# Performance work log

Hardware: AMD Instinct MI355X
Metric: run time of the kernel (lower is better)

The kernel has to match this reference:

```python
import jax, jax.numpy as jnp
import numpy as np
from jax import lax

DIM = 256
HEADS = 8
SR = 4
EPS = 1e-5
SCALE = (DIM // HEADS) ** -0.5


def _dwconv(x, wgt, stride, pad):
    # x: (B,C,H,W), wgt: (C,1,kh,kw) depthwise
    return lax.conv_general_dilated(
        x, wgt, (stride, stride), [(pad, pad), (pad, pad)],
        feature_group_count=x.shape[1],
        dimension_numbers=("NCHW", "OIHW", "NCHW"))


def _bn(x, g, b, m, v):
    # eval-mode batchnorm folded to per-channel scale/shift
    s = g / jnp.sqrt(v + EPS)
    return x * s[:, None, None] + (b - m * s)[:, None, None]


def setup_inputs() -> dict:
    key = jax.random.key(0)
    ks = jax.random.split(key, 16)
    b, h, w = 8, 64, 64
    c = DIM
    n = h * w

    def rn(k, shape, s=0.05):
        return jax.random.normal(k, shape, jnp.float32) * s

    return dict(
        x=jax.random.normal(ks[0], (b, n, c), jnp.float32),
        h=h, w=w,
        Wq=rn(ks[1], (c, c)), bq=rn(ks[2], (c,)),
        Wkv=rn(ks[3], (2 * c, c)), bkv=rn(ks[4], (2 * c,)),
        sr_w1=rn(ks[5], (c, 1, SR + 3, SR + 3), 0.1),
        bn1_gamma=1.0 + rn(ks[6], (c,)), bn1_beta=rn(ks[7], (c,)),
        bn1_mean=rn(ks[8], (c,)), bn1_var=jnp.abs(1.0 + rn(ks[9], (c,))),
        sr_w2=1.0 + rn(ks[10], (c,), 0.2),  # 1x1 depthwise conv == per-channel scale
        bn2_gamma=1.0 + rn(ks[11], (c,)), bn2_beta=rn(ks[12], (c,)),
        bn2_mean=rn(ks[13], (c,)), bn2_var=jnp.abs(1.0 + rn(ks[14], (c,))),
        local_w=rn(ks[15], (c, 1, 3, 3), 0.1),
        local_b=jnp.zeros((c,), jnp.float32),
    )


def reference(x, h, w, Wq, bq, Wkv, bkv, sr_w1, bn1_gamma, bn1_beta, bn1_mean,
              bn1_var, sr_w2, bn2_gamma, bn2_beta, bn2_mean, bn2_var,
              local_w, local_b):
    b, n, c = x.shape
    hd = c // HEADS
    xi = x.transpose(0, 2, 1).reshape(b, c, h, w)  # (b,c,h,w)

    # q projection (1x1 conv == channel matmul)
    q = jnp.einsum("bchw,dc->bdhw", xi, Wq) + bq[None, :, None, None]
    q = q.reshape(b, HEADS, hd, n).transpose(0, 1, 3, 2)  # (b,H,n,hd)

    # spatial reduction: dwconv7 s4 + BN + GELU + dw1x1 + BN
    kv = _dwconv(xi, sr_w1, SR, (SR + 3) // 2)
    kv = _bn(kv, bn1_gamma, bn1_beta, bn1_mean, bn1_var)
    kv = jax.nn.gelu(kv, approximate=False)
    kv = kv * sr_w2[None, :, None, None]
    kv = _bn(kv, bn2_gamma, bn2_beta, bn2_mean, bn2_var)

    # residual local depthwise 3x3 conv
    kv = _dwconv(kv, local_w, 1, 1) + local_b[None, :, None, None] + kv

    # kv projection and split
    kvp = jnp.einsum("bchw,dc->bdhw", kv, Wkv) + bkv[None, :, None, None]
    k_, v_ = jnp.split(kvp, 2, axis=1)
    m = k_.shape[2] * k_.shape[3]
    k_ = k_.reshape(b, HEADS, hd, m)                       # (b,H,hd,m)
    v_ = v_.reshape(b, HEADS, hd, m).transpose(0, 1, 3, 2)  # (b,H,m,hd)

    attn = jax.nn.softmax(jnp.einsum("bhnd,bhdm->bhnm", q, k_) * SCALE, axis=-1)
    out = jnp.einsum("bhnm,bhmd->bhnd", attn, v_)           # (b,H,n,hd)
    out = out.transpose(0, 1, 3, 2).reshape(b, c, n).transpose(0, 2, 1)
    return out
```

## Files before the change

### kernel.cpp

```cpp
#include <hip/hip_runtime.h>
#include <math.h>

typedef __bf16 bf16;
typedef bf16 bf16x4 __attribute__((ext_vector_type(4)));
typedef bf16 bf16x8 __attribute__((ext_vector_type(8)));
typedef float f32x4 __attribute__((ext_vector_type(4)));

static_assert(sizeof(bf16x8) == 16, "bf16x8 must be 16B");

#define QSCALE (0.17677669529663687f * 1.4426950408889634f)
#define NEGBIG (-1e30f)

__device__ __forceinline__ f32x4 mfma16(bf16x8 a, bf16x8 b, f32x4 c) {
  return __builtin_amdgcn_mfma_f32_16x16x32_bf16(a, b, c, 0, 0, 0);
}


__global__ __launch_bounds__(256) void k_cvt(
    const float* __restrict__ Wq, const float* __restrict__ Wkv,
    const float* __restrict__ w7, bf16* __restrict__ Wqb,
    bf16* __restrict__ Wkvb, float* __restrict__ w7t) {
  const int tid = threadIdx.x;
  const int blk = blockIdx.x;
  if (blk < 96) {
    const float* src;
    bf16* dst;
    if (blk < 32) {
      const int idx = blk * 256 + tid;
      src = Wq + (size_t)idx * 8;
      dst = Wqb + (size_t)idx * 8;
    } else {
      const int idx = (blk - 32) * 256 + tid;
      src = Wkv + (size_t)idx * 8;
      dst = Wkvb + (size_t)idx * 8;
    }
    const float4 a = ((const float4*)src)[0];
    const float4 b = ((const float4*)src)[1];
    bf16x8 r;
    r[0] = (bf16)a.x; r[1] = (bf16)a.y; r[2] = (bf16)a.z; r[3] = (bf16)a.w;
    r[4] = (bf16)b.x; r[5] = (bf16)b.y; r[6] = (bf16)b.z; r[7] = (bf16)b.w;
    *(bf16x8*)dst = r;
  } else {
    const int c = tid;
    #pragma unroll
    for (int tap = 0; tap < 49; tap++)
      w7t[tap * 256 + c] = w7[c * 49 + tap];
  }
}

__global__ __launch_bounds__(256) void k_sr(
    const float* __restrict__ x, const float* __restrict__ w7t,
    const float* __restrict__ g1, const float* __restrict__ b1,
    const float* __restrict__ m1, const float* __restrict__ v1,
    const float* __restrict__ sw2,
    const float* __restrict__ g2, const float* __restrict__ b2,
    const float* __restrict__ m2, const float* __restrict__ v2,
    bf16* __restrict__ kv1) {
  __shared__ float part[4][256];
  const int tid = threadIdx.x;
  const int team = tid >> 6, g = tid & 63;
  const int c0 = g * 4;
  const int blk = blockIdx.x;
  const int b = blk & 7, m = blk >> 3;
  const int oy = m >> 4, ox = m & 15;

  float4 xv[13], wv[13];
  float msk[13];
  #pragma unroll
  for (int j = 0; j < 13; j++) {
    const int tap = team + j * 4;
    const int ky = tap / 7, kx = tap - ky * 7;
    const int iy = oy * 4 - 3 + ky, ix = ox * 4 - 3 + kx;
    msk[j] = (tap < 49 && iy >= 0 && iy < 64 && ix >= 0 && ix < 64) ? 1.f : 0.f;
    const int iyc = iy < 0 ? 0 : (iy > 63 ? 63 : iy);
    const int ixc = ix < 0 ? 0 : (ix > 63 ? 63 : ix);
    const int tc = tap > 48 ? 48 : tap;
    xv[j] = *(const float4*)(x + ((size_t)b * 4096 + iyc * 64 + ixc) * 256 + c0);
    wv[j] = *(const float4*)(w7t + tc * 256 + c0);
  }
  float a0 = 0.f, a1 = 0.f, a2 = 0.f, a3 = 0.f;
  #pragma unroll
  for (int j = 0; j < 13; j++) {
    a0 += xv[j].x * wv[j].x * msk[j];
    a1 += xv[j].y * wv[j].y * msk[j];
    a2 += xv[j].z * wv[j].z * msk[j];
    a3 += xv[j].w * wv[j].w * msk[j];
  }
  *(f32x4*)&part[team][c0] = (f32x4){a0, a1, a2, a3};
  __syncthreads();
  const int c = tid;
  float y = part[0][c] + part[1][c] + part[2][c] + part[3][c];
  float s = g1[c] / sqrtf(v1[c] + 1e-5f);
  y = y * s + (b1[c] - m1[c] * s);
  y = 0.5f * y * (1.f + erff(y * 0.70710678118654752f));
  y *= sw2[c];
  s = g2[c] / sqrtf(v2[c] + 1e-5f);
  y = y * s + (b2[c] - m2[c] * s);
  kv1[((size_t)b * 256 + m) * 256 + c] = (bf16)y;
}

__global__ __launch_bounds__(256) void k_local(
    const bf16* __restrict__ kv1, const float* __restrict__ w3,
    const float* __restrict__ lb, bf16* __restrict__ kv2) {
  const int c = threadIdx.x;
  const int m = blockIdx.x;
  const int b = blockIdx.y;
  const int oy = m >> 4, ox = m & 15;
  float acc = 0.f;
  #pragma unroll
  for (int ky = 0; ky < 3; ky++) {
    const int iy = oy - 1 + ky;
    if (iy < 0 || iy >= 16) continue;
    #pragma unroll
    for (int kx = 0; kx < 3; kx++) {
      const int ix = ox - 1 + kx;
      if (ix < 0 || ix >= 16) continue;
      acc += (float)kv1[((size_t)b * 256 + iy * 16 + ix) * 256 + c] *
             w3[c * 9 + ky * 3 + kx];
    }
  }
  const float center = (float)kv1[((size_t)b * 256 + m) * 256 + c];
  kv2[((size_t)b * 256 + m) * 256 + c] = (bf16)(acc + lb[c] + center);
}

__global__ __launch_bounds__(256) void k_kvproj(
    const bf16* __restrict__ kv2, const bf16* __restrict__ Wkvb,
    const float* __restrict__ bkv, bf16* __restrict__ k_a,
    bf16* __restrict__ v_b) {
  __shared__ float rows[8][256];
  const int tid = threadIdx.x;
  const int mt = blockIdx.x;
  const int b = blockIdx.y;
  const bf16* src = kv2 + ((size_t)b * 256 + mt * 8) * 256;
  {
    const bf16x8 v = *(const bf16x8*)(src + tid * 8);
    const int r0 = tid >> 5, cc = (tid * 8) & 255;
    #pragma unroll
    for (int k = 0; k < 8; k++) rows[r0][cc + k] = (float)v[k];
  }
  __syncthreads();

  float acck[8] = {0}, accv[8] = {0};
  for (int oc = 0; oc < 32; oc++) {
    const bf16x8 w0 = *(const bf16x8*)(Wkvb + (size_t)tid * 256 + oc * 8);
    const bf16x8 w1 = *(const bf16x8*)(Wkvb + ((size_t)tid + 256) * 256 + oc * 8);
    float wf0[8], wf1[8];
    #pragma unroll
    for (int j = 0; j < 8; j++) { wf0[j] = (float)w0[j]; wf1[j] = (float)w1[j]; }
    #pragma unroll
    for (int r = 0; r < 8; r++) {
      const float4* rp = (const float4*)&rows[r][oc * 8];
      const float4 ra = rp[0], rb = rp[1];
      const float rv[8] = {ra.x, ra.y, ra.z, ra.w, rb.x, rb.y, rb.z, rb.w};
      #pragma unroll
      for (int j = 0; j < 8; j++) {
        acck[r] += wf0[j] * rv[j];
        accv[r] += wf1[j] * rv[j];
      }
    }
  }
  const float bk = bkv[tid], bv = bkv[tid + 256];
  const int h = tid >> 5, d = tid & 31;
  #pragma unroll
  for (int r = 0; r < 8; r++) {
    const int m = mt * 8 + r;
    k_a[(((size_t)b * 8 + h) * 256 + m) * 32 + d] = (bf16)(acck[r] + bk);
    v_b[(((size_t)b * 8 + h) * 32 + d) * 256 + m] = (bf16)(accv[r] + bv);
  }
}

__global__ __launch_bounds__(256) void k_qproj(
    const float* __restrict__ x, const bf16* __restrict__ Wqb,
    const float* __restrict__ bq, char* __restrict__ qout) {
  __shared__ bf16 xs[32 * 264];
  const int tid = threadIdx.x, wv = tid >> 6, lane = tid & 63;
  const int qd = lane >> 4, l15 = lane & 15;
  const size_t rowbase = (size_t)blockIdx.x * 32;

  #pragma unroll
  for (int it = 0; it < 4; it++) {
    const int idx = it * 256 + tid;
    const int lr = idx >> 5, pos = idx & 31;
    const float* src = x + (rowbase + lr) * 256 + pos * 8;
    const float4 a = ((const float4*)src)[0];
    const float4 b = ((const float4*)src)[1];
    bf16x8 r;
    r[0] = (bf16)a.x; r[1] = (bf16)a.y; r[2] = (bf16)a.z; r[3] = (bf16)a.w;
    r[4] = (bf16)b.x; r[5] = (bf16)b.y; r[6] = (bf16)b.z; r[7] = (bf16)b.w;
    *(bf16x8*)(xs + lr * 264 + pos * 8) = r;
  }
  __syncthreads();

  const int rowhalf = wv & 1, colhalf = wv >> 1;
  f32x4 acc[8];
  #pragma unroll
  for (int dt = 0; dt < 8; dt++) acc[dt] = (f32x4){0.f, 0.f, 0.f, 0.f};

  for (int kc = 0; kc < 8; kc++) {
    const bf16x8 a = *(const bf16x8*)(xs + (rowhalf * 16 + l15) * 264 +
                                      kc * 32 + qd * 8);
    #pragma unroll
    for (int dt = 0; dt < 8; dt++) {
      const int d = colhalf * 128 + dt * 16 + l15;
      const bf16x8 bb = *(const bf16x8*)(Wqb + (size_t)d * 256 + kc * 32 + qd * 8);
      acc[dt] = mfma16(a, bb, acc[dt]);
    }
  }
  #pragma unroll
  for (int dt = 0; dt < 8; dt++) {
    const int d = colhalf * 128 + dt * 16 + l15;
    const float bias = bq[d];
    #pragma unroll
    for (int r = 0; r < 4; r++) {
      const size_t row = rowbase + rowhalf * 16 + qd * 4 + r;
      *(bf16*)(qout + row * 1024 + (d >> 5) * 128 + (size_t)(d & 31) * 2) =
          (bf16)((acc[dt][r] + bias) * QSCALE);
    }
  }
}

__global__ __launch_bounds__(256) void k_attn(
    char* __restrict__ qo, const bf16* __restrict__ k_a,
    const bf16* __restrict__ v_b) {
  float* out = (float*)qo;
  const int tid = threadIdx.x;
  const int wv = tid >> 6, lane = tid & 63;
  const int qd = lane >> 4, l15 = lane & 15;
  const int b = blockIdx.z, h = blockIdx.y;
  const int bh = b * 8 + h;
  const int n_base = blockIdx.x * 256 + wv * 64;

  const char* qb = qo + (size_t)(b * 4096 + n_base) * 1024 + h * 128;
  bf16x8 qf[4];
  #pragma unroll
  for (int qi = 0; qi < 4; qi++)
    qf[qi] = *(const bf16x8*)(qb + (size_t)(qi * 16 + l15) * 1024 + qd * 16);

  const bf16* kb = k_a + (size_t)bh * 256 * 32;
  const bf16* vb = v_b + (size_t)bh * 32 * 256;

  f32x4 acc[4][2];
  float mr[4], lr[4];
  #pragma unroll
  for (int qi = 0; qi < 4; qi++) {
    acc[qi][0] = (f32x4){0.f, 0.f, 0.f, 0.f};
    acc[qi][1] = (f32x4){0.f, 0.f, 0.f, 0.f};
    mr[qi] = NEGBIG;
    lr[qi] = 0.f;
  }
  const int kperm = 8 * (l15 >> 2) + (l15 & 3);

  for (int ch = 0; ch < 8; ch++) {
    const bf16x8 ka0 = *(const bf16x8*)(kb + (size_t)(ch * 32 + kperm) * 32 + qd * 8);
    const bf16x8 ka1 = *(const bf16x8*)(kb + (size_t)(ch * 32 + kperm + 4) * 32 + qd * 8);
    const bf16x8 va0 = *(const bf16x8*)(vb + (size_t)l15 * 256 + ch * 32 + qd * 8);
    const bf16x8 va1 = *(const bf16x8*)(vb + (size_t)(16 + l15) * 256 + ch * 32 + qd * 8);
    const f32x4 z = (f32x4){0.f, 0.f, 0.f, 0.f};
    #pragma unroll
    for (int qi = 0; qi < 4; qi++) {
      f32x4 s0 = mfma16(ka0, qf[qi], z);
      f32x4 s1 = mfma16(ka1, qf[qi], z);
      float mx = fmaxf(fmaxf(fmaxf(s0[0], s0[1]), fmaxf(s0[2], s0[3])),
                       fmaxf(fmaxf(s1[0], s1[1]), fmaxf(s1[2], s1[3])));
      mx = fmaxf(mx, __shfl_xor(mx, 16, 64));
      mx = fmaxf(mx, __shfl_xor(mx, 32, 64));
      const float mn = fmaxf(mr[qi], mx);
      const float alpha = __builtin_amdgcn_exp2f(mr[qi] - mn);
      mr[qi] = mn;
      float p[8], ls = 0.f;
      #pragma unroll
      for (int j = 0; j < 4; j++) { p[j] = __builtin_amdgcn_exp2f(s0[j] - mn); ls += p[j]; }
      #pragma unroll
      for (int j = 0; j < 4; j++) { p[4 + j] = __builtin_amdgcn_exp2f(s1[j] - mn); ls += p[4 + j]; }
      lr[qi] = lr[qi] * alpha + ls;
      bf16x8 pb;
      #pragma unroll
      for (int j = 0; j < 8; j++) pb[j] = (bf16)p[j];
      #pragma unroll
      for (int r = 0; r < 4; r++) { acc[qi][0][r] *= alpha; acc[qi][1][r] *= alpha; }
      acc[qi][0] = mfma16(va0, pb, acc[qi][0]);
      acc[qi][1] = mfma16(va1, pb, acc[qi][1]);
    }
  }
  #pragma unroll
  for (int qi = 0; qi < 4; qi++) {
    float l = lr[qi];
    l += __shfl_xor(l, 16, 64);
    l += __shfl_xor(l, 32, 64);
    const float inv = 1.f / l;
    const int nn = n_base + qi * 16 + l15;
    float* ob = out + (size_t)(b * 4096 + nn) * 256 + h * 32;
    #pragma unroll
    for (int t = 0; t < 2; t++) {
      *(float4*)(ob + t * 16 + qd * 4) =
          (float4){acc[qi][t][0] * inv, acc[qi][t][1] * inv,
                   acc[qi][t][2] * inv, acc[qi][t][3] * inv};
    }
  }
}

extern "C" void kernel_launch(void* const* d_in, const int* in_sizes, int n_in,
                              void* d_out, int out_size, void* d_ws, size_t ws_size,
                              hipStream_t stream) {
  const float* x      = (const float*)d_in[0];
  const float* Wq     = (const float*)d_in[3];
  const float* bq     = (const float*)d_in[4];
  const float* Wkv    = (const float*)d_in[5];
  const float* bkv    = (const float*)d_in[6];
  const float* sr_w1  = (const float*)d_in[7];
  const float* bn1_g  = (const float*)d_in[8];
  const float* bn1_b  = (const float*)d_in[9];
  const float* bn1_m  = (const float*)d_in[10];
  const float* bn1_v  = (const float*)d_in[11];
  const float* sw2    = (const float*)d_in[12];
  const float* bn2_g  = (const float*)d_in[13];
  const float* bn2_b  = (const float*)d_in[14];
  const float* bn2_m  = (const float*)d_in[15];
  const float* bn2_v  = (const float*)d_in[16];
  const float* lw     = (const float*)d_in[17];
  const float* lb     = (const float*)d_in[18];

  const int B = in_sizes[0] / (4096 * 256);

  bf16* Wqb  = (bf16*)d_ws;
  bf16* Wkvb = Wqb + 65536;
  float* w7t = (float*)(Wkvb + 131072);
  bf16* kv1  = (bf16*)(w7t + 12544);
  bf16* kv2  = kv1 + (size_t)B * 256 * 256;
  bf16* k_a  = kv2 + (size_t)B * 256 * 256;
  bf16* v_b  = k_a + (size_t)B * 8 * 256 * 32;

  char* dx = (char*)d_out;

  k_cvt<<<dim3(97), 256, 0, stream>>>(Wq, Wkv, sr_w1, Wqb, Wkvb, w7t);
  k_sr<<<dim3(256 * B), 256, 0, stream>>>(x, w7t, bn1_g, bn1_b, bn1_m, bn1_v,
                                          sw2, bn2_g, bn2_b, bn2_m, bn2_v, kv1);
  k_local<<<dim3(256, B), 256, 0, stream>>>(kv1, lw, lb, kv2);
  k_kvproj<<<dim3(32, B), 256, 0, stream>>>(kv2, Wkvb, bkv, k_a, v_b);
  k_qproj<<<dim3(B * 128), 256, 0, stream>>>(x, Wqb, bq, dx);
  k_attn<<<dim3(16, 8, B), 256, 0, stream>>>(dx, k_a, v_b);
}
```

Before: 216.0 us.

## Fuse local dwconv into kv projection, retile q-proj, prefetch K/V in attention

Merges the 3x3 depthwise local conv into the kv projection kernel, staging a halo tile in shared memory. This removes one launch and the kv2 intermediate round trip. The q-projection warp tiling changes so each warp covers 32 rows by 64 columns, reusing each Wq fragment across two MFMAs. The attention loop now loads the next chunk's K/V fragments before computing the current one, to hide load latency. The fused kernel still runs only 32×B blocks, so the conv work gets less parallelism.

New measurement: 195.3 us. 9.5% less time.

```diff
diff --git a/kernel.cpp b/kernel.cpp
--- a/kernel.cpp
+++ b/kernel.cpp
@@ -99,47 +99,46 @@
   kv1[((size_t)b * 256 + m) * 256 + c] = (bf16)y;
 }
 
-__global__ __launch_bounds__(256) void k_local(
+__global__ __launch_bounds__(256) void k_localkv(
     const bf16* __restrict__ kv1, const float* __restrict__ w3,
-    const float* __restrict__ lb, bf16* __restrict__ kv2) {
-  const int c = threadIdx.x;
-  const int m = blockIdx.x;
-  const int b = blockIdx.y;
-  const int oy = m >> 4, ox = m & 15;
-  float acc = 0.f;
-  #pragma unroll
-  for (int ky = 0; ky < 3; ky++) {
-    const int iy = oy - 1 + ky;
-    if (iy < 0 || iy >= 16) continue;
-    #pragma unroll
-    for (int kx = 0; kx < 3; kx++) {
-      const int ix = ox - 1 + kx;
-      if (ix < 0 || ix >= 16) continue;
-      acc += (float)kv1[((size_t)b * 256 + iy * 16 + ix) * 256 + c] *
-             w3[c * 9 + ky * 3 + kx];
-    }
-  }
-  const float center = (float)kv1[((size_t)b * 256 + m) * 256 + c];
-  kv2[((size_t)b * 256 + m) * 256 + c] = (bf16)(acc + lb[c] + center);
-}
-
-__global__ __launch_bounds__(256) void k_kvproj(
-    const bf16* __restrict__ kv2, const bf16* __restrict__ Wkvb,
+    const float* __restrict__ lb, const bf16* __restrict__ Wkvb,
     const float* __restrict__ bkv, bf16* __restrict__ k_a,
     bf16* __restrict__ v_b) {
+  __shared__ bf16 halo[3][10][256];
   __shared__ float rows[8][256];
-  const int tid = threadIdx.x;
+  const int c = threadIdx.x;
   const int mt = blockIdx.x;
   const int b = blockIdx.y;
-  const bf16* src = kv2 + ((size_t)b * 256 + mt * 8) * 256;
-  {
-    const bf16x8 v = *(const bf16x8*)(src + tid * 8);
-    const int r0 = tid >> 5, cc = (tid * 8) & 255;
-    #pragma unroll
-    for (int k = 0; k < 8; k++) rows[r0][cc + k] = (float)v[k];
-  }
+  const int oy = mt >> 1, o0 = (mt & 1) * 8;
+
+  #pragma unroll
+  for (int p = 0; p < 30; p++) {
+    const int dy = p / 10, xi = p - dy * 10;
+    const int iy = oy - 1 + dy, ix = o0 - 1 + xi;
+    const bool ok = (iy >= 0 && iy < 16 && ix >= 0 && ix < 16);
+    const int iyc = ok ? iy : 0, ixc = ok ? ix : 0;
+    const bf16 v = kv1[((size_t)b * 256 + iyc * 16 + ixc) * 256 + c];
+    halo[dy][xi][c] = ok ? v : (bf16)0.f;
+  }
+  float w3f[9];
+  #pragma unroll
+  for (int t = 0; t < 9; t++) w3f[t] = w3[c * 9 + t];
+  const float lbf = lb[c];
   __syncthreads();
 
+  #pragma unroll
+  for (int r = 0; r < 8; r++) {
+    float acc = lbf + (float)halo[1][r + 1][c];
+    #pragma unroll
+    for (int ky = 0; ky < 3; ky++)
+      #pragma unroll
+      for (int kx = 0; kx < 3; kx++)
+        acc += (float)halo[ky][r + kx][c] * w3f[ky * 3 + kx];
+    rows[r][c] = acc;
+  }
+  __syncthreads();
+
+  const int tid = c;
   float acck[8] = {0}, accv[8] = {0};
   for (int oc = 0; oc < 32; oc++) {
     const bf16x8 w0 = *(const bf16x8*)(Wkvb + (size_t)tid * 256 + oc * 8);
@@ -163,7 +162,7 @@
   const int h = tid >> 5, d = tid & 31;
   #pragma unroll
   for (int r = 0; r < 8; r++) {
-    const int m = mt * 8 + r;
+    const int m = (oy * 16 + o0) + r;
     k_a[(((size_t)b * 8 + h) * 256 + m) * 32 + d] = (bf16)(acck[r] + bk);
     v_b[(((size_t)b * 8 + h) * 32 + d) * 256 + m] = (bf16)(accv[r] + bv);
   }
@@ -191,30 +190,36 @@
   }
   __syncthreads();
 
-  const int rowhalf = wv & 1, colhalf = wv >> 1;
-  f32x4 acc[8];
-  #pragma unroll
-  for (int dt = 0; dt < 8; dt++) acc[dt] = (f32x4){0.f, 0.f, 0.f, 0.f};
-
+  f32x4 acc0[4], acc1[4];
+  #pragma unroll
+  for (int dt = 0; dt < 4; dt++) {
+    acc0[dt] = (f32x4){0.f, 0.f, 0.f, 0.f};
+    acc1[dt] = (f32x4){0.f, 0.f, 0.f, 0.f};
+  }
+  #pragma unroll 2
   for (int kc = 0; kc < 8; kc++) {
-    const bf16x8 a = *(const bf16x8*)(xs + (rowhalf * 16 + l15) * 264 +
-                                      kc * 32 + qd * 8);
-    #pragma unroll
-    for (int dt = 0; dt < 8; dt++) {
-      const int d = colhalf * 128 + dt * 16 + l15;
+    const bf16x8 a0 = *(const bf16x8*)(xs + l15 * 264 + kc * 32 + qd * 8);
+    const bf16x8 a1 = *(const bf16x8*)(xs + (16 + l15) * 264 + kc * 32 + qd * 8);
+    #pragma unroll
+    for (int dt = 0; dt < 4; dt++) {
+      const int d = wv * 64 + dt * 16 + l15;
       const bf16x8 bb = *(const bf16x8*)(Wqb + (size_t)d * 256 + kc * 32 + qd * 8);
-      acc[dt] = mfma16(a, bb, acc[dt]);
-    }
-  }
-  #pragma unroll
-  for (int dt = 0; dt < 8; dt++) {
-    const int d = colhalf * 128 + dt * 16 + l15;
+      acc0[dt] = mfma16(a0, bb, acc0[dt]);
+      acc1[dt] = mfma16(a1, bb, acc1[dt]);
+    }
+  }
+  #pragma unroll
+  for (int dt = 0; dt < 4; dt++) {
+    const int d = wv * 64 + dt * 16 + l15;
     const float bias = bq[d];
     #pragma unroll
     for (int r = 0; r < 4; r++) {
-      const size_t row = rowbase + rowhalf * 16 + qd * 4 + r;
-      *(bf16*)(qout + row * 1024 + (d >> 5) * 128 + (size_t)(d & 31) * 2) =
-          (bf16)((acc[dt][r] + bias) * QSCALE);
+      const size_t row0 = rowbase + qd * 4 + r;
+      const size_t row1 = rowbase + 16 + qd * 4 + r;
+      *(bf16*)(qout + row0 * 1024 + (d >> 5) * 128 + (size_t)(d & 31) * 2) =
+          (bf16)((acc0[dt][r] + bias) * QSCALE);
+      *(bf16*)(qout + row1 * 1024 + (d >> 5) * 128 + (size_t)(d & 31) * 2) =
+          (bf16)((acc1[dt][r] + bias) * QSCALE);
     }
   }
 }
@@ -250,11 +255,17 @@
   }
   const int kperm = 8 * (l15 >> 2) + (l15 & 3);
 
+  bf16x8 ka0 = *(const bf16x8*)(kb + (size_t)kperm * 32 + qd * 8);
+  bf16x8 ka1 = *(const bf16x8*)(kb + (size_t)(kperm + 4) * 32 + qd * 8);
+  bf16x8 va0 = *(const bf16x8*)(vb + (size_t)l15 * 256 + qd * 8);
+  bf16x8 va1 = *(const bf16x8*)(vb + (size_t)(16 + l15) * 256 + qd * 8);
+
   for (int ch = 0; ch < 8; ch++) {
-    const bf16x8 ka0 = *(const bf16x8*)(kb + (size_t)(ch * 32 + kperm) * 32 + qd * 8);
-    const bf16x8 ka1 = *(const bf16x8*)(kb + (size_t)(ch * 32 + kperm + 4) * 32 + qd * 8);
-    const bf16x8 va0 = *(const bf16x8*)(vb + (size_t)l15 * 256 + ch * 32 + qd * 8);
-    const bf16x8 va1 = *(const bf16x8*)(vb + (size_t)(16 + l15) * 256 + ch * 32 + qd * 8);
+    const int cn = (ch < 7 ? ch + 1 : 7) * 32;
+    const bf16x8 nk0 = *(const bf16x8*)(kb + (size_t)(cn + kperm) * 32 + qd * 8);
+    const bf16x8 nk1 = *(const bf16x8*)(kb + (size_t)(cn + kperm + 4) * 32 + qd * 8);
+    const bf16x8 nv0 = *(const bf16x8*)(vb + (size_t)l15 * 256 + cn + qd * 8);
+    const bf16x8 nv1 = *(const bf16x8*)(vb + (size_t)(16 + l15) * 256 + cn + qd * 8);
     const f32x4 z = (f32x4){0.f, 0.f, 0.f, 0.f};
     #pragma unroll
     for (int qi = 0; qi < 4; qi++) {
@@ -281,6 +292,7 @@
       acc[qi][0] = mfma16(va0, pb, acc[qi][0]);
       acc[qi][1] = mfma16(va1, pb, acc[qi][1]);
     }
+    ka0 = nk0; ka1 = nk1; va0 = nv0; va1 = nv1;
   }
   #pragma unroll
   for (int qi = 0; qi < 4; qi++) {
@@ -326,8 +338,7 @@
   bf16* Wkvb = Wqb + 65536;
   float* w7t = (float*)(Wkvb + 131072);
   bf16* kv1  = (bf16*)(w7t + 12544);
-  bf16* kv2  = kv1 + (size_t)B * 256 * 256;
-  bf16* k_a  = kv2 + (size_t)B * 256 * 256;
+  bf16* k_a  = kv1 + (size_t)B * 256 * 256;
   bf16* v_b  = k_a + (size_t)B * 8 * 256 * 32;
 
   char* dx = (char*)d_out;
@@ -335,8 +346,7 @@
   k_cvt<<<dim3(97), 256, 0, stream>>>(Wq, Wkv, sr_w1, Wqb, Wkvb, w7t);
   k_sr<<<dim3(256 * B), 256, 0, stream>>>(x, w7t, bn1_g, bn1_b, bn1_m, bn1_v,
                                           sw2, bn2_g, bn2_b, bn2_m, bn2_v, kv1);
-  k_local<<<dim3(256, B), 256, 0, stream>>>(kv1, lw, lb, kv2);
-  k_kvproj<<<dim3(32, B), 256, 0, stream>>>(kv2, Wkvb, bkv, k_a, v_b);
+  k_localkv<<<dim3(32, B), 256, 0, stream>>>(kv1, lw, lb, Wkvb, bkv, k_a, v_b);
   k_qproj<<<dim3(B * 128), 256, 0, stream>>>(x, Wqb, bq, dx);
   k_attn<<<dim3(16, 8, B), 256, 0, stream>>>(dx, k_a, v_b);
 }
```
